# Performance work log

Hardware: AMD Instinct MI355X
Metric: run time of the kernel (lower is better)

## Reference

```python
import jax, jax.numpy as jnp
import numpy as np

B, C, H, W = 4, 64, 256, 256
DS = 4        # ClusterLocalAtt downscale
CS = 2        # FastClusterAtt cluster_stride
NH = 4        # FastClusterAtt num_heads
G = 4         # OrthoConvClustering groups
N_NOISE = 8   # number of -1 (noise) labels; even and divisible by B


def _maxpool(x, k):
    b, c, h, w = x.shape
    return x.reshape(b, c, h // k, k, w // k, k).max(axis=(3, 5))


def _normalize(x, eps=1e-12):
    n = jnp.linalg.norm(x, axis=-1, keepdims=True)
    return x / jnp.maximum(n, eps)


def _feat_sim(cf, nf):
    # cf: (B,k,HW), nf: (B,n,HW) -> (B,k) mean cosine similarity over noise rows
    return jnp.einsum('bkl,bnl->bkn', _normalize(cf), _normalize(nf)).mean(-1)


def setup_inputs():
    key = jax.random.key(0)
    ks = jax.random.split(key, 12)
    x = jax.random.normal(ks[0], (B, C, H, W), jnp.float32)
    noise_idx = jnp.arange(N_NOISE, dtype=jnp.int32)
    labels = jax.random.randint(ks[1], (B * C,), 0, 12, dtype=jnp.int32)
    labels = labels.at[noise_idx].set(-1)
    inv = 1.0 / np.sqrt(C // G)
    return {
        'x': x, 'labels': labels, 'noise_idx': noise_idx,
        'qkv_w1': jax.random.normal(ks[2], (3 * C,), jnp.float32) * 0.5,
        'qkv_b1': jax.random.normal(ks[3], (3 * C,), jnp.float32) * 0.1,
        'up_k': jax.random.normal(ks[4], (C, DS, DS), jnp.float32) * 0.25,
        'up_b': jax.random.normal(ks[5], (C,), jnp.float32) * 0.1,
        'clu_w': jax.random.normal(ks[6], (G, C // G, C // G), jnp.float32) * inv,
        'clu_b': jnp.zeros((C,), jnp.float32),
        'qkv_w2': jax.random.normal(ks[7], (3 * C,), jnp.float32) * 0.5,
        'bais_w': jax.random.normal(ks[8], (C, C), jnp.float32) * (inv * 0.5),
        'bais_b': jax.random.normal(ks[9], (C,), jnp.float32) * 0.1,
    }


def reference(x, labels, noise_idx, qkv_w1, qkv_b1, up_k, up_b,
              clu_w, clu_b, qkv_w2, bais_w, bais_b):
    idx3 = jnp.arange(3 * C) // 3  # grouped 1x1 conv (groups=C): out ch j reads in ch j//3
    # ================= ClusterLocalAtt =================
    x_down = _maxpool(x, DS)                        # (B,C,Hd,Wd)
    Hd, Wd = H // DS, W // DS
    hw = Hd * Wd
    qkv = x_down[:, idx3] * qkv_w1[None, :, None, None] + qkv_b1[None, :, None, None]
    qkv = qkv.reshape(3 * B * C, hw)                # torch: reshape(1, 3*B*C, hw)
    q, k, v = jnp.split(qkv, 3, axis=0)             # each (B*C, hw) - batch/ch mixed, faithful
    valid = labels != -1
    allowed = (labels[:, None] == labels[None, :]) & valid[:, None] & valid[None, :]
    scores = q @ k.T                                # (BC, BC)
    attn = jax.nn.softmax(jnp.where(allowed, scores, -1e30), axis=-1)
    att = jnp.where(valid[:, None], attn @ v, 0.0)  # noise rows stay zero
    out = att.reshape(B, C, Hd, Wd)
    # depthwise ConvTranspose2d(kernel=DS, stride=DS): each input px -> DSxDS block
    up = jnp.einsum('bchw,cpq->bchpwq', out, up_k).reshape(B, C, H, W)
    up = up + up_b[None, :, None, None]
    noise = x.reshape(B * C, H * W)[noise_idx].reshape(B, N_NOISE // B, H * W)
    sim = _feat_sim(up.reshape(B, C, H * W), noise)[:, :, None, None]  # (B,C,1,1)
    out_clu = x + (up + (1.0 - sim) * x)
    # ================= FastClusterAtt =================
    xf = out_clu.reshape(B, G, C // G, H * W)
    xc = jnp.einsum('goi,bgil->bgol', clu_w, xf).reshape(B, C, H * W) + clu_b[None, :, None]
    x_ds = _maxpool(xc.reshape(B, C, H, W), CS)     # (B,C,Hs,Ws)
    Hs, Ws = H // CS, W // CS
    Ls = Hs * Ws
    qkv2 = (x_ds[:, idx3] * qkv_w2[None, :, None, None]).reshape(B, 3, NH, C // NH, Ls)
    qh, kh, vh = qkv2[:, 0], qkv2[:, 1], qkv2[:, 2]  # (B,NH,hd,Ls)
    sc = (qh * kh).sum(axis=2, keepdims=True) / np.sqrt(C // NH)  # (B,NH,1,Ls)
    a = jax.nn.softmax(sc, axis=-1)
    oh = (a * vh).sum(axis=-1).reshape(B, C)        # (B,C) global pooled heads
    # bilinear upsample of a spatially-constant map is the same constant -> skip interp
    ov = jnp.einsum('oc,bc->bo', bais_w, oh) + bais_b
    out_full = jnp.broadcast_to(ov[:, :, None, None], (B, C, H, W))
    sim2 = _feat_sim(out_full.reshape(B, C, H * W), noise)[:, :, None, None]
    WWT = jnp.einsum('goi,gpi->gop', clu_w, clu_w)
    I = jnp.eye(C // G, dtype=clu_w.dtype)
    ortho = 1.0 - jax.lax.stop_gradient(jnp.mean((WWT - I) ** 2))
    out2 = out_full * (1.0 - sim2) + ortho * out_clu
    return out_clu + out2
```

## Files before the change

### kernel.cpp

```cpp
#include <hip/hip_runtime.h>
#include <math.h>

#define WS_XD     0u
#define WS_S      1048576u
#define WS_GPART  1048832u
#define WS_COEF   2113792u
#define WS_CONST  2138368u
#define WS_ATT    2138624u
#define WS_FAC    3187200u
#define WS_XDS    3187456u
#define WS_ALPHA  7382016u
#define WS_BETA   7382272u
#define WS_NSTAT  7382273u
#define WS_P2     7382304u

__device__ __forceinline__ float bsum(float v, float* sd, int tid) {
    sd[tid] = v; __syncthreads();
    for (int off = 128; off > 0; off >>= 1) {
        if (tid < off) sd[tid] += sd[tid + off];
        __syncthreads();
    }
    float r = sd[0]; __syncthreads(); return r;
}
__device__ __forceinline__ float bmax(float v, float* sd, int tid) {
    sd[tid] = v; __syncthreads();
    for (int off = 128; off > 0; off >>= 1) {
        if (tid < off) sd[tid] = fmaxf(sd[tid], sd[tid + off]);
        __syncthreads();
    }
    float r = sd[0]; __syncthreads(); return r;
}

template <bool ISN>
__device__ __forceinline__ void pool4_body(const float4* __restrict__ xr,
                                           float* __restrict__ xd, int tid,
                                           float& sum, float& s, float& ss) {
    for (int it = 0; it < 16; ++it) {
        int o = it * 256 + tid;
        int h = o >> 6, w = o & 63;
        float m = -INFINITY;
        #pragma unroll
        for (int p = 0; p < 4; ++p) {
            float4 v = xr[(4 * h + p) * 64 + w];
            m = fmaxf(m, fmaxf(fmaxf(v.x, v.y), fmaxf(v.z, v.w)));
            if (ISN) {
                s  += v.x + v.y + v.z + v.w;
                ss += v.x*v.x + v.y*v.y + v.z*v.z + v.w*v.w;
            }
        }
        xd[o] = m; sum += m;
    }
}

__global__ __launch_bounds__(256) void k_pool4(const float* __restrict__ x,
                                               const int* __restrict__ nidx,
                                               float* __restrict__ ws) {
    __shared__ float sd[256];
    int r = blockIdx.x, tid = threadIdx.x;
    const float4* xr = (const float4*)x + (size_t)r * 16384;
    float* xd = ws + WS_XD + (size_t)r * 4096;
    bool isn = false;
    #pragma unroll
    for (int n = 0; n < 8; ++n) isn = isn || (nidx[n] == r);
    float sum = 0.f, s = 0.f, ss = 0.f;
    if (isn) pool4_body<true>(xr, xd, tid, sum, s, ss);
    else     pool4_body<false>(xr, xd, tid, sum, s, ss);
    float st = bsum(sum, sd, tid);
    if (tid == 0) ws[WS_S + r] = st;
    if (isn) {
        float ts = bsum(s, sd, tid);
        float tss = bsum(ss, sd, tid);
        if (tid == 0) {
            for (int n = 0; n < 8; ++n)
                if (nidx[n] == r) { ws[WS_NSTAT + n] = ts; ws[WS_NSTAT + 8 + n] = sqrtf(tss); }
        }
    }
}

__global__ __launch_bounds__(256) void k_gram(float* __restrict__ ws) {
    __shared__ __align__(16) float As[64][68];
    __shared__ __align__(16) float Bs[64][68];
    int tid = threadIdx.x, tx = tid & 15, ty = tid >> 4;
    int ra0 = blockIdx.y * 64, rb0 = 80 + blockIdx.x * 64, k0 = blockIdx.z * 64;
    const float4* xd4 = (const float4*)(ws + WS_XD);
    #pragma unroll
    for (int q = 0; q < 4; ++q) {
        int idx = q * 256 + tid;
        int row = idx >> 4, cf = idx & 15;
        float4 a = xd4[(size_t)(ra0 + row) * 1024 + (k0 >> 2) + cf];
        As[cf*4+0][row] = a.x; As[cf*4+1][row] = a.y; As[cf*4+2][row] = a.z; As[cf*4+3][row] = a.w;
        float4 b = xd4[(size_t)(rb0 + row) * 1024 + (k0 >> 2) + cf];
        Bs[cf*4+0][row] = b.x; Bs[cf*4+1][row] = b.y; Bs[cf*4+2][row] = b.z; Bs[cf*4+3][row] = b.w;
    }
    __syncthreads();
    float acc[4][4] = {};
    #pragma unroll 4
    for (int kk = 0; kk < 64; ++kk) {
        float4 a = *(const float4*)&As[kk][ty * 4];
        float4 b = *(const float4*)&Bs[kk][tx * 4];
        acc[0][0] += a.x*b.x; acc[0][1] += a.x*b.y; acc[0][2] += a.x*b.z; acc[0][3] += a.x*b.w;
        acc[1][0] += a.y*b.x; acc[1][1] += a.y*b.y; acc[1][2] += a.y*b.z; acc[1][3] += a.y*b.w;
        acc[2][0] += a.z*b.x; acc[2][1] += a.z*b.y; acc[2][2] += a.z*b.z; acc[2][3] += a.z*b.w;
        acc[3][0] += a.w*b.x; acc[3][1] += a.w*b.y; acc[3][2] += a.w*b.z; acc[3][3] += a.w*b.w;
    }
    float* gp = ws + WS_GPART + (size_t)blockIdx.z * 16384;
    #pragma unroll
    for (int i = 0; i < 4; ++i) {
        float4 o = make_float4(acc[i][0], acc[i][1], acc[i][2], acc[i][3]);
        *(float4*)&gp[(size_t)(ra0 + ty * 4 + i) * 128 + blockIdx.x * 64 + tx * 4] = o;
    }
}

__global__ __launch_bounds__(256) void k_attn1(const int* __restrict__ labels,
                                               const float* __restrict__ w1,
                                               const float* __restrict__ b1,
                                               float* __restrict__ ws) {
    __shared__ float sd[256];
    __shared__ float attn_s[256];
    __shared__ float grow[128];
    int i = blockIdx.x, tid = threadIdx.x;
    int labi = labels[i];
    bool validi = (labi != -1);
    int bi = (i >= 192) ? 1 : 0;
    int ji = i - bi * 192;
    int rq = bi * 64 + ji / 3;
    if (tid < 128) {
        const float* gp = ws + WS_GPART + (size_t)rq * 128 + tid;
        float acc = 0.f;
        #pragma unroll 8
        for (int p = 0; p < 64; ++p) acc += gp[(size_t)p * 16384];
        grow[tid] = acc;
    }
    __syncthreads();
    float wq = w1[ji], bq = b1[ji];
    int gk = 256 + tid;
    int bk = (gk >= 384) ? 2 : 1;
    int jk = gk - bk * 192;
    int rk = bk * 64 + jk / 3;
    float wk = w1[jk], bbk = b1[jk];
    int labj = labels[tid];
    bool allowed = validi && (labj == labi) && (labj != -1);
    float score = wq * wk * grow[rk - 80]
                + wq * bbk * ws[WS_S + rq]
                + wk * bq  * ws[WS_S + rk]
                + 4096.0f * bq * bbk;
    float sc = allowed ? score : -1e30f;
    float m = bmax(sc, sd, tid);
    float e = __expf(sc - m);
    float Z = bsum(e, sd, tid);
    float attn = validi ? (e / Z) : 0.0f;
    attn_s[tid] = attn;
    int gv = 512 + tid;
    int bv = (gv >= 576) ? 3 : 2;
    int jv = gv - bv * 192;
    float csum = bsum(attn * b1[jv], sd, tid);
    if (tid < 96) {
        float s = 0.0f;
        if (tid < 86) {
            int rv = 170 + tid;
            int lo, hi, jadd;
            if (rv < 192) { int c = rv - 128; lo = 3 * c; if (lo < 128) lo = 128; hi = 3 * c + 2; jadd = -128; }
            else          { int c = rv - 192; lo = 3 * c; hi = 3 * c + 2; jadd = 64; }
            for (int jj = lo; jj <= hi; ++jj) s += attn_s[jj + jadd] * w1[jj];
        }
        ws[WS_COEF + i * 96 + tid] = s;
    }
    if (tid == 0) ws[WS_CONST + i] = csum;
}

__global__ __launch_bounds__(256) void k_attmm(float* __restrict__ ws) {
    __shared__ __align__(16) float As[96][68];
    __shared__ __align__(16) float Bs[96][64];
    int tid = threadIdx.x, tx = tid & 15, ty = tid >> 4;
    int col0 = blockIdx.x * 64, row0 = blockIdx.y * 64;
    const float4* cf4 = (const float4*)(ws + WS_COEF);
    const float4* xd4 = (const float4*)(ws + WS_XD);
    #pragma unroll
    for (int q = 0; q < 6; ++q) {
        int f = q * 256 + tid;
        {
            int row = f / 24, c24 = f - row * 24;
            float4 v = cf4[(size_t)(row0 + row) * 24 + c24];
            As[c24*4+0][row] = v.x; As[c24*4+1][row] = v.y; As[c24*4+2][row] = v.z; As[c24*4+3][row] = v.w;
        }
        {
            int row = f >> 4, c16 = f & 15;
            float4 v = make_float4(0.f, 0.f, 0.f, 0.f);
            if (row < 86) v = xd4[(size_t)(170 + row) * 1024 + (col0 >> 2) + c16];
            *(float4*)&Bs[row][c16 * 4] = v;
        }
    }
    __syncthreads();
    float acc[4][4] = {};
    #pragma unroll 4
    for (int kk = 0; kk < 96; ++kk) {
        float4 a = *(const float4*)&As[kk][ty * 4];
        float4 b = *(const float4*)&Bs[kk][tx * 4];
        acc[0][0] += a.x*b.x; acc[0][1] += a.x*b.y; acc[0][2] += a.x*b.z; acc[0][3] += a.x*b.w;
        acc[1][0] += a.y*b.x; acc[1][1] += a.y*b.y; acc[1][2] += a.y*b.z; acc[1][3] += a.y*b.w;
        acc[2][0] += a.z*b.x; acc[2][1] += a.z*b.y; acc[2][2] += a.z*b.z; acc[2][3] += a.z*b.w;
        acc[3][0] += a.w*b.x; acc[3][1] += a.w*b.y; acc[3][2] += a.w*b.z; acc[3][3] += a.w*b.w;
    }
    float* att = ws + WS_ATT;
    #pragma unroll
    for (int i = 0; i < 4; ++i) {
        int row = row0 + ty * 4 + i;
        float cv = ws[WS_CONST + row];
        float4 o = make_float4(acc[i][0] + cv, acc[i][1] + cv, acc[i][2] + cv, acc[i][3] + cv);
        *(float4*)&att[(size_t)row * 4096 + col0 + tx * 4] = o;
    }
}

__global__ __launch_bounds__(256) void k_sim(const float* __restrict__ x,
                                             const int* __restrict__ nidx,
                                             const float* __restrict__ upk,
                                             const float* __restrict__ upb,
                                             float* __restrict__ ws) {
    __shared__ float sd[768];
    int r = blockIdx.x, tid = threadIdx.x;
    int b = r >> 6, c = r & 63;
    const float* att = ws + WS_ATT + (size_t)r * 4096;
    const float4* xn0 = (const float4*)x + (size_t)nidx[2 * b] * 16384;
    const float4* xn1 = (const float4*)x + (size_t)nidx[2 * b + 1] * 16384;
    const float4* k4p = (const float4*)upk + c * 4;
    float ub = upb[c];
    float4 kk0 = k4p[0], kk1 = k4p[1], kk2 = k4p[2], kk3 = k4p[3];
    float s2 = 0.f, d0 = 0.f, d1 = 0.f;
    for (int it = 0; it < 64; ++it) {
        int f = it * 256 + tid;
        int rowf = f >> 6, c4 = f & 63;
        float av = att[(rowf >> 2) * 64 + c4];
        int p = rowf & 3;
        float4 kv = (p == 0) ? kk0 : ((p == 1) ? kk1 : ((p == 2) ? kk2 : kk3));
        float4 a0 = xn0[f], a1 = xn1[f];
        float u;
        u = av * kv.x + ub; s2 += u * u; d0 += u * a0.x; d1 += u * a1.x;
        u = av * kv.y + ub; s2 += u * u; d0 += u * a0.y; d1 += u * a1.y;
        u = av * kv.z + ub; s2 += u * u; d0 += u * a0.z; d1 += u * a1.z;
        u = av * kv.w + ub; s2 += u * u; d0 += u * a0.w; d1 += u * a1.w;
    }
    sd[tid] = s2; sd[256 + tid] = d0; sd[512 + tid] = d1;
    __syncthreads();
    for (int off = 128; off > 0; off >>= 1) {
        if (tid < off) {
            sd[tid]       += sd[tid + off];
            sd[256 + tid] += sd[256 + tid + off];
            sd[512 + tid] += sd[512 + tid + off];
        }
        __syncthreads();
    }
    if (tid == 0) {
        float nup = fmaxf(sqrtf(sd[0]), 1e-12f);
        float n0 = fmaxf(ws[WS_NSTAT + 8 + 2 * b], 1e-12f);
        float n1 = fmaxf(ws[WS_NSTAT + 8 + 2 * b + 1], 1e-12f);
        float sim = 0.5f * (sd[256] / (nup * n0) + sd[512] / (nup * n1));
        ws[WS_FAC + r] = 2.0f - sim;
    }
}

__global__ __launch_bounds__(128) void k_cluds(const float* __restrict__ x,
                                               const float* __restrict__ upk,
                                               const float* __restrict__ upb,
                                               const float* __restrict__ cw,
                                               const float* __restrict__ cb,
                                               float* __restrict__ ws) {
    __shared__ float wcl[256];
    __shared__ float kup[256];
    __shared__ float cbl[16], ubl[16], fcl[16];
    __shared__ float atile[16][64];
    int h2 = blockIdx.x, g = blockIdx.y, b = blockIdx.z;
    int t = threadIdx.x;
    wcl[t] = cw[g * 256 + t];       wcl[t + 128] = cw[g * 256 + t + 128];
    kup[t] = upk[g * 256 + t];      kup[t + 128] = upk[g * 256 + t + 128];
    if (t < 16) {
        cbl[t] = cb[g * 16 + t];
        ubl[t] = upb[g * 16 + t];
        fcl[t] = ws[WS_FAC + b * 64 + g * 16 + t];
    }
    int h_att = h2 >> 1;
    {
        int ch = t >> 3, cb4 = (t & 7) * 8;
        const float4* arow = (const float4*)(ws + WS_ATT + (size_t)(b * 64 + g * 16 + ch) * 4096 + h_att * 64 + cb4);
        float4 v0 = arow[0], v1 = arow[1];
        *(float4*)&atile[ch][cb4] = v0;
        *(float4*)&atile[ch][cb4 + 4] = v1;
    }
    __syncthreads();
    int r0 = 2 * h2;
    int p0 = r0 & 3;
    int q0 = (2 * t) & 3;
    int wa = t >> 1;
    float oc[16][4];
    #pragma unroll
    for (int i = 0; i < 16; ++i) {
        int ch = g * 16 + i;
        float av = atile[i][wa];
        const float* xc = x + (size_t)(b * 64 + ch) * 65536;
        float2 x0 = *(const float2*)&xc[r0 * 256 + 2 * t];
        float2 x1 = *(const float2*)&xc[(r0 + 1) * 256 + 2 * t];
        float ub = ubl[i], fc = fcl[i];
        oc[i][0] = av * kup[i * 16 + p0 * 4 + q0]           + ub + fc * x0.x;
        oc[i][1] = av * kup[i * 16 + p0 * 4 + q0 + 1]       + ub + fc * x0.y;
        oc[i][2] = av * kup[i * 16 + (p0 + 1) * 4 + q0]     + ub + fc * x1.x;
        oc[i][3] = av * kup[i * 16 + (p0 + 1) * 4 + q0 + 1] + ub + fc * x1.y;
    }
    float* xds = ws + WS_XDS;
    #pragma unroll
    for (int o = 0; o < 16; ++o) {
        float cbv = cbl[o];
        float a0 = cbv, a1 = cbv, a2 = cbv, a3 = cbv;
        #pragma unroll
        for (int i = 0; i < 16; ++i) {
            float wv = wcl[o * 16 + i];
            a0 += wv * oc[i][0]; a1 += wv * oc[i][1];
            a2 += wv * oc[i][2]; a3 += wv * oc[i][3];
        }
        float m = fmaxf(fmaxf(a0, a1), fmaxf(a2, a3));
        xds[(size_t)((b * 64 + g * 16 + o) * 128 + h2) * 128 + t] = m;
    }
}

__global__ __launch_bounds__(256) void k_attn2a(const float* __restrict__ w2,
                                                float* __restrict__ ws) {
    __shared__ float wl2[192];
    __shared__ float ms[256], dsh[256];
    __shared__ float ns[256][17];
    int chunk = blockIdx.x, nh = blockIdx.y, b = blockIdx.z, tid = threadIdx.x;
    if (tid < 192) wl2[tid] = w2[tid];
    __syncthreads();
    const float4* X4 = (const float4*)(ws + WS_XDS + (size_t)b * 1048576);
    int li = chunk * 256 + tid;
    float4 sc = make_float4(0.f, 0.f, 0.f, 0.f);
    #pragma unroll
    for (int d = 0; d < 16; ++d) {
        int jq = nh * 16 + d, jk = 64 + nh * 16 + d;
        float4 q4 = X4[(size_t)(jq / 3) * 4096 + li];
        float4 k4 = X4[(size_t)(jk / 3) * 4096 + li];
        float wqk = wl2[jq] * wl2[jk] * 0.25f;
        sc.x += wqk * q4.x * k4.x; sc.y += wqk * q4.y * k4.y;
        sc.z += wqk * q4.z * k4.z; sc.w += wqk * q4.w * k4.w;
    }
    float m = fmaxf(fmaxf(sc.x, sc.y), fmaxf(sc.z, sc.w));
    float p0 = __expf(sc.x - m), p1 = __expf(sc.y - m), p2 = __expf(sc.z - m), p3 = __expf(sc.w - m);
    float den = p0 + p1 + p2 + p3;
    float num[16];
    #pragma unroll
    for (int d = 0; d < 16; ++d) {
        int jv = 128 + nh * 16 + d;
        float4 v4 = X4[(size_t)(jv / 3) * 4096 + li];
        num[d] = wl2[jv] * (p0 * v4.x + p1 * v4.y + p2 * v4.z + p3 * v4.w);
    }
    ms[tid] = m; dsh[tid] = den;
    #pragma unroll
    for (int d = 0; d < 16; ++d) ns[tid][d] = num[d];
    __syncthreads();
    for (int off = 128; off > 0; off >>= 1) {
        if (tid < off) {
            float ma = ms[tid], mb = ms[tid + off];
            float M = fmaxf(ma, mb);
            float ra = __expf(ma - M), rb = __expf(mb - M);
            dsh[tid] = dsh[tid] * ra + dsh[tid + off] * rb;
            #pragma unroll
            for (int d = 0; d < 16; ++d)
                ns[tid][d] = ns[tid][d] * ra + ns[tid + off][d] * rb;
            ms[tid] = M;
        }
        __syncthreads();
    }
    if (tid == 0) {
        float* p = ws + WS_P2 + ((size_t)(b * 4 + nh) * 16 + chunk) * 18;
        p[0] = ms[0]; p[1] = dsh[0];
        #pragma unroll
        for (int d = 0; d < 16; ++d) p[2 + d] = ns[0][d];
    }
}

__global__ __launch_bounds__(256) void k_tail(const float* __restrict__ bw,
                                              const float* __restrict__ bb,
                                              const float* __restrict__ cw,
                                              float* __restrict__ ws) {
    __shared__ float ohs[256], sd[256];
    int tid = threadIdx.x;
    int grp = tid >> 4;
    int j = tid & 15;
    const float* p = ws + WS_P2 + ((size_t)grp * 16 + j) * 18;
    float m = p[0], den = p[1], num[16];
    #pragma unroll
    for (int d = 0; d < 16; ++d) num[d] = p[2 + d];
    #pragma unroll
    for (int mask = 1; mask <= 8; mask <<= 1) {
        float mo = __shfl_xor(m, mask);
        float dn = __shfl_xor(den, mask);
        float M = fmaxf(m, mo);
        float ra = __expf(m - M), rb = __expf(mo - M);
        den = den * ra + dn * rb;
        #pragma unroll
        for (int d = 0; d < 16; ++d)
            num[d] = num[d] * ra + __shfl_xor(num[d], mask) * rb;
        m = M;
    }
    if (j == 0) {
        int b = grp >> 2, nh = grp & 3;
        #pragma unroll
        for (int d = 0; d < 16; ++d) ohs[b * 64 + nh * 16 + d] = num[d] / den;
    }
    __syncthreads();
    int b = tid >> 6, o = tid & 63;
    float s = bb[o];
    #pragma unroll 4
    for (int c2 = 0; c2 < 64; ++c2) s += bw[o * 64 + c2] * ohs[b * 64 + c2];
    float oacc = 0.f;
    for (int u = 0; u < 4; ++u) {
        int e = tid * 4 + u;
        int g = e >> 8, oo = (e >> 4) & 15, pp = e & 15;
        float ssv = 0.f;
        #pragma unroll
        for (int i = 0; i < 16; ++i) ssv += cw[g * 256 + oo * 16 + i] * cw[g * 256 + pp * 16 + i];
        float dd = ssv - ((oo == pp) ? 1.0f : 0.0f);
        oacc += dd * dd;
    }
    float tot = bsum(oacc, sd, tid);
    float nd = fmaxf(fabsf(s) * 256.0f, 1e-12f);
    float t0 = ws[WS_NSTAT + 2 * b], t1 = ws[WS_NSTAT + 2 * b + 1];
    float n0 = fmaxf(ws[WS_NSTAT + 8 + 2 * b], 1e-12f);
    float n1 = fmaxf(ws[WS_NSTAT + 8 + 2 * b + 1], 1e-12f);
    float sim2 = (s / nd) * 0.5f * (t0 / n0 + t1 / n1);
    ws[WS_ALPHA + tid] = (1.0f - sim2) * s;
    if (tid == 0) ws[WS_BETA] = 2.0f - tot / 1024.0f;
}

__global__ __launch_bounds__(256) void k_final(const float* __restrict__ x,
                                               const float* __restrict__ upk,
                                               const float* __restrict__ upb,
                                               const float* __restrict__ ws,
                                               float* __restrict__ out) {
    int idx = blockIdx.x * 256 + threadIdx.x;
    int r = idx >> 14;
    int rem = idx & 16383;
    int rowf = rem >> 6, c4 = rem & 63;
    int c = r & 63;
    float av = ws[WS_ATT + (size_t)r * 4096 + (rowf >> 2) * 64 + c4];
    int p = rowf & 3;
    float4 kv = ((const float4*)upk)[c * 4 + p];
    float ub = upb[c];
    float fac = ws[WS_FAC + r], al = ws[WS_ALPHA + r], be = ws[WS_BETA];
    float4 xv = ((const float4*)x)[idx];
    float4 o;
    o.x = be * (av * kv.x + ub + fac * xv.x) + al;
    o.y = be * (av * kv.y + ub + fac * xv.y) + al;
    o.z = be * (av * kv.z + ub + fac * xv.z) + al;
    o.w = be * (av * kv.w + ub + fac * xv.w) + al;
    ((float4*)out)[idx] = o;
}

extern "C" void kernel_launch(void* const* d_in, const int* in_sizes, int n_in,
                              void* d_out, int out_size, void* d_ws, size_t ws_size,
                              hipStream_t stream) {
    const float* x      = (const float*)d_in[0];
    const int*   labels = (const int*)d_in[1];
    const int*   nidx   = (const int*)d_in[2];
    const float* w1     = (const float*)d_in[3];
    const float* b1     = (const float*)d_in[4];
    const float* upk    = (const float*)d_in[5];
    const float* upb    = (const float*)d_in[6];
    const float* cw     = (const float*)d_in[7];
    const float* cb     = (const float*)d_in[8];
    const float* w2     = (const float*)d_in[9];
    const float* bw     = (const float*)d_in[10];
    const float* bb     = (const float*)d_in[11];
    float* ws  = (float*)d_ws;
    float* out = (float*)d_out;

    hipLaunchKernelGGL(k_pool4,  dim3(256),        dim3(256), 0, stream, x, nidx, ws);
    hipLaunchKernelGGL(k_gram,   dim3(2, 2, 64),   dim3(256), 0, stream, ws);
    hipLaunchKernelGGL(k_attn1,  dim3(256),        dim3(256), 0, stream, labels, w1, b1, ws);
    hipLaunchKernelGGL(k_attmm,  dim3(64, 4),      dim3(256), 0, stream, ws);
    hipLaunchKernelGGL(k_sim,    dim3(256),        dim3(256), 0, stream, x, nidx, upk, upb, ws);
    hipLaunchKernelGGL(k_cluds,  dim3(128, 4, 4),  dim3(128), 0, stream, x, upk, upb, cw, cb, ws);
    hipLaunchKernelGGL(k_attn2a, dim3(16, 4, 4),   dim3(256), 0, stream, w2, ws);
    hipLaunchKernelGGL(k_tail,   dim3(1),          dim3(256), 0, stream, bw, bb, cw, ws);
    hipLaunchKernelGGL(k_final,  dim3(16384),      dim3(256), 0, stream, x, upk, upb, ws, out);
}
```

Measured before the change: 111.4 us.

## Fuse noise-similarity partial sums into attention matmul epilogue, drop k_sim kernel

The separate k_sim kernel, which reread the attention map and noise channels, is removed. Its per-channel norm and dot products are now computed in the k_attmm epilogue from values still in registers, using per-tile partial sums written to workspace. k_cluds reduces those 64 partials per row to form the similarity factor. This saves a launch and a reread of the attention map, at the cost of a heavier matmul epilogue, extra workspace traffic, and reusing the WS_GPART region (WS_SIMP aliases it).

New measurement: 108.7 us. 2.4% less time.

```diff
diff --git a/kernel.cpp b/kernel.cpp
--- a/kernel.cpp
+++ b/kernel.cpp
@@ -4,6 +4,7 @@
 #define WS_XD     0u
 #define WS_S      1048576u
 #define WS_GPART  1048832u
+#define WS_SIMP   1048832u
 #define WS_COEF   2113792u
 #define WS_CONST  2138368u
 #define WS_ATT    2138624u
@@ -168,13 +169,22 @@
     if (tid == 0) ws[WS_CONST + i] = csum;
 }
 
-__global__ __launch_bounds__(256) void k_attmm(float* __restrict__ ws) {
+__global__ __launch_bounds__(256) void k_attmm(const float* __restrict__ x,
+                                               const int* __restrict__ nidx,
+                                               const float* __restrict__ upk,
+                                               const float* __restrict__ upb,
+                                               float* __restrict__ ws) {
     __shared__ __align__(16) float As[96][68];
     __shared__ __align__(16) float Bs[96][64];
+    __shared__ __align__(16) float kup[64][16];
+    __shared__ float ubl[64];
     int tid = threadIdx.x, tx = tid & 15, ty = tid >> 4;
     int col0 = blockIdx.x * 64, row0 = blockIdx.y * 64;
+    int b = blockIdx.y;
     const float4* cf4 = (const float4*)(ws + WS_COEF);
     const float4* xd4 = (const float4*)(ws + WS_XD);
+    ((float4*)kup)[tid] = ((const float4*)upk)[tid];
+    if (tid < 64) ubl[tid] = upb[tid];
     #pragma unroll
     for (int q = 0; q < 6; ++q) {
         int f = q * 256 + tid;
@@ -195,66 +205,63 @@
     #pragma unroll 4
     for (int kk = 0; kk < 96; ++kk) {
         float4 a = *(const float4*)&As[kk][ty * 4];
-        float4 b = *(const float4*)&Bs[kk][tx * 4];
-        acc[0][0] += a.x*b.x; acc[0][1] += a.x*b.y; acc[0][2] += a.x*b.z; acc[0][3] += a.x*b.w;
-        acc[1][0] += a.y*b.x; acc[1][1] += a.y*b.y; acc[1][2] += a.y*b.z; acc[1][3] += a.y*b.w;
-        acc[2][0] += a.z*b.x; acc[2][1] += a.z*b.y; acc[2][2] += a.z*b.z; acc[2][3] += a.z*b.w;
-        acc[3][0] += a.w*b.x; acc[3][1] += a.w*b.y; acc[3][2] += a.w*b.z; acc[3][3] += a.w*b.w;
+        float4 bq = *(const float4*)&Bs[kk][tx * 4];
+        acc[0][0] += a.x*bq.x; acc[0][1] += a.x*bq.y; acc[0][2] += a.x*bq.z; acc[0][3] += a.x*bq.w;
+        acc[1][0] += a.y*bq.x; acc[1][1] += a.y*bq.y; acc[1][2] += a.y*bq.z; acc[1][3] += a.y*bq.w;
+        acc[2][0] += a.z*bq.x; acc[2][1] += a.z*bq.y; acc[2][2] += a.z*bq.z; acc[2][3] += a.z*bq.w;
+        acc[3][0] += a.w*bq.x; acc[3][1] += a.w*bq.y; acc[3][2] += a.w*bq.z; acc[3][3] += a.w*bq.w;
     }
     float* att = ws + WS_ATT;
+    float avv[4][4];
     #pragma unroll
     for (int i = 0; i < 4; ++i) {
         int row = row0 + ty * 4 + i;
         float cv = ws[WS_CONST + row];
-        float4 o = make_float4(acc[i][0] + cv, acc[i][1] + cv, acc[i][2] + cv, acc[i][3] + cv);
+        avv[i][0] = acc[i][0] + cv; avv[i][1] = acc[i][1] + cv;
+        avv[i][2] = acc[i][2] + cv; avv[i][3] = acc[i][3] + cv;
+        float4 o = make_float4(avv[i][0], avv[i][1], avv[i][2], avv[i][3]);
         *(float4*)&att[(size_t)row * 4096 + col0 + tx * 4] = o;
     }
-}
-
-__global__ __launch_bounds__(256) void k_sim(const float* __restrict__ x,
-                                             const int* __restrict__ nidx,
-                                             const float* __restrict__ upk,
-                                             const float* __restrict__ upb,
-                                             float* __restrict__ ws) {
-    __shared__ float sd[768];
-    int r = blockIdx.x, tid = threadIdx.x;
-    int b = r >> 6, c = r & 63;
-    const float* att = ws + WS_ATT + (size_t)r * 4096;
-    const float4* xn0 = (const float4*)x + (size_t)nidx[2 * b] * 16384;
-    const float4* xn1 = (const float4*)x + (size_t)nidx[2 * b + 1] * 16384;
-    const float4* k4p = (const float4*)upk + c * 4;
-    float ub = upb[c];
-    float4 kk0 = k4p[0], kk1 = k4p[1], kk2 = k4p[2], kk3 = k4p[3];
-    float s2 = 0.f, d0 = 0.f, d1 = 0.f;
-    for (int it = 0; it < 64; ++it) {
-        int f = it * 256 + tid;
-        int rowf = f >> 6, c4 = f & 63;
-        float av = att[(rowf >> 2) * 64 + c4];
-        int p = rowf & 3;
-        float4 kv = (p == 0) ? kk0 : ((p == 1) ? kk1 : ((p == 2) ? kk2 : kk3));
-        float4 a0 = xn0[f], a1 = xn1[f];
-        float u;
-        u = av * kv.x + ub; s2 += u * u; d0 += u * a0.x; d1 += u * a1.x;
-        u = av * kv.y + ub; s2 += u * u; d0 += u * a0.y; d1 += u * a1.y;
-        u = av * kv.z + ub; s2 += u * u; d0 += u * a0.z; d1 += u * a1.z;
-        u = av * kv.w + ub; s2 += u * u; d0 += u * a0.w; d1 += u * a1.w;
-    }
-    sd[tid] = s2; sd[256 + tid] = d0; sd[512 + tid] = d1;
-    __syncthreads();
-    for (int off = 128; off > 0; off >>= 1) {
-        if (tid < off) {
-            sd[tid]       += sd[tid + off];
-            sd[256 + tid] += sd[256 + tid + off];
-            sd[512 + tid] += sd[512 + tid + off];
-        }
-        __syncthreads();
-    }
-    if (tid == 0) {
-        float nup = fmaxf(sqrtf(sd[0]), 1e-12f);
-        float n0 = fmaxf(ws[WS_NSTAT + 8 + 2 * b], 1e-12f);
-        float n1 = fmaxf(ws[WS_NSTAT + 8 + 2 * b + 1], 1e-12f);
-        float sim = 0.5f * (sd[256] / (nup * n0) + sd[512] / (nup * n1));
-        ws[WS_FAC + r] = 2.0f - sim;
+    const float* xn0 = x + (size_t)nidx[2 * b] * 65536;
+    const float* xn1 = x + (size_t)nidx[2 * b + 1] * 65536;
+    float s2[4] = {}, d0[4] = {}, d1[4] = {};
+    #pragma unroll
+    for (int j = 0; j < 4; ++j) {
+        int hw = col0 + tx * 4 + j;
+        int h = hw >> 6, wc = hw & 63;
+        #pragma unroll
+        for (int p = 0; p < 4; ++p) {
+            float4 a0 = *(const float4*)&xn0[(4 * h + p) * 256 + 4 * wc];
+            float4 a1 = *(const float4*)&xn1[(4 * h + p) * 256 + 4 * wc];
+            #pragma unroll
+            for (int i = 0; i < 4; ++i) {
+                int c = ty * 4 + i;
+                float av = avv[i][j], ub = ubl[c];
+                float u;
+                u = av * kup[c][p * 4 + 0] + ub; s2[i] += u*u; d0[i] += u*a0.x; d1[i] += u*a1.x;
+                u = av * kup[c][p * 4 + 1] + ub; s2[i] += u*u; d0[i] += u*a0.y; d1[i] += u*a1.y;
+                u = av * kup[c][p * 4 + 2] + ub; s2[i] += u*u; d0[i] += u*a0.z; d1[i] += u*a1.z;
+                u = av * kup[c][p * 4 + 3] + ub; s2[i] += u*u; d0[i] += u*a0.w; d1[i] += u*a1.w;
+            }
+        }
+    }
+    #pragma unroll
+    for (int mask = 1; mask <= 8; mask <<= 1) {
+        #pragma unroll
+        for (int i = 0; i < 4; ++i) {
+            s2[i] += __shfl_xor(s2[i], mask);
+            d0[i] += __shfl_xor(d0[i], mask);
+            d1[i] += __shfl_xor(d1[i], mask);
+        }
+    }
+    if (tx == 0) {
+        #pragma unroll
+        for (int i = 0; i < 4; ++i) {
+            int row = row0 + ty * 4 + i;
+            ws[WS_SIMP +          (size_t)row * 64 + blockIdx.x] = s2[i];
+            ws[WS_SIMP + 16384 +  (size_t)row * 64 + blockIdx.x] = d0[i];
+            ws[WS_SIMP + 32768 +  (size_t)row * 64 + blockIdx.x] = d1[i];
+        }
     }
 }
 
@@ -275,7 +282,24 @@
     if (t < 16) {
         cbl[t] = cb[g * 16 + t];
         ubl[t] = upb[g * 16 + t];
-        fcl[t] = ws[WS_FAC + b * 64 + g * 16 + t];
+        int row = b * 64 + g * 16 + t;
+        const float4* sp0 = (const float4*)(ws + WS_SIMP + (size_t)row * 64);
+        const float4* sp1 = (const float4*)(ws + WS_SIMP + 16384 + (size_t)row * 64);
+        const float4* sp2 = (const float4*)(ws + WS_SIMP + 32768 + (size_t)row * 64);
+        float s2 = 0.f, d0 = 0.f, d1 = 0.f;
+        #pragma unroll
+        for (int cb4 = 0; cb4 < 16; ++cb4) {
+            float4 v0 = sp0[cb4], v1 = sp1[cb4], v2 = sp2[cb4];
+            s2 += v0.x + v0.y + v0.z + v0.w;
+            d0 += v1.x + v1.y + v1.z + v1.w;
+            d1 += v2.x + v2.y + v2.z + v2.w;
+        }
+        float nup = fmaxf(sqrtf(s2), 1e-12f);
+        float n0 = fmaxf(ws[WS_NSTAT + 8 + 2 * b], 1e-12f);
+        float n1 = fmaxf(ws[WS_NSTAT + 8 + 2 * b + 1], 1e-12f);
+        float fac = 2.0f - 0.5f * (d0 / (nup * n0) + d1 / (nup * n1));
+        fcl[t] = fac;
+        ws[WS_FAC + row] = fac;
     }
     int h_att = h2 >> 1;
     {
@@ -474,8 +498,7 @@
     hipLaunchKernelGGL(k_pool4,  dim3(256),        dim3(256), 0, stream, x, nidx, ws);
     hipLaunchKernelGGL(k_gram,   dim3(2, 2, 64),   dim3(256), 0, stream, ws);
     hipLaunchKernelGGL(k_attn1,  dim3(256),        dim3(256), 0, stream, labels, w1, b1, ws);
-    hipLaunchKernelGGL(k_attmm,  dim3(64, 4),      dim3(256), 0, stream, ws);
-    hipLaunchKernelGGL(k_sim,    dim3(256),        dim3(256), 0, stream, x, nidx, upk, upb, ws);
+    hipLaunchKernelGGL(k_attmm,  dim3(64, 4),      dim3(256), 0, stream, x, nidx, upk, upb, ws);
     hipLaunchKernelGGL(k_cluds,  dim3(128, 4, 4),  dim3(128), 0, stream, x, upk, upb, cw, cb, ws);
     hipLaunchKernelGGL(k_attn2a, dim3(16, 4, 4),   dim3(256), 0, stream, w2, ws);
     hipLaunchKernelGGL(k_tail,   dim3(1),          dim3(256), 0, stream, bw, bb, cw, ws);
```
